# Kernel optimization log

Measured on AMD Instinct MI355X. Metric: run time of the kernel, lower is better.

Reference implementation:

```python
import jax, jax.numpy as jnp
import numpy as np

H_DIM, W_DIM, D_MODEL = 128, 128, 1024
N_HEADS, HEAD_DIM = 16, 64


def setup_inputs() -> dict:
    key = jax.random.key(0)
    ks = jax.random.split(key, 8)
    s = D_MODEL ** -0.5
    return {
        "hidden_state": jax.random.normal(ks[0], (H_DIM, W_DIM, D_MODEL), jnp.float32),
        "attn_mask": jnp.zeros((1, 1, W_DIM, W_DIM), jnp.float32),
        "cos": jax.random.uniform(ks[1], (H_DIM, W_DIM, 1, HEAD_DIM), jnp.float32),
        "sin": jax.random.uniform(ks[2], (H_DIM, W_DIM, 1, HEAD_DIM), jnp.float32),
        "Wq": jax.random.normal(ks[3], (D_MODEL, N_HEADS * HEAD_DIM), jnp.float32) * s,
        "Wk": jax.random.normal(ks[4], (D_MODEL, N_HEADS * HEAD_DIM), jnp.float32) * s,
        "Wv": jax.random.normal(ks[5], (D_MODEL, N_HEADS * HEAD_DIM), jnp.float32) * s,
        "Wo": jax.random.normal(ks[6], (2 * D_MODEL, D_MODEL), jnp.float32) * s,
    }


def _rotate_half(x):
    x1, x2 = jnp.split(x, 2, axis=-1)
    return jnp.concatenate((-x2, x1), axis=-1)


def reference(hidden_state, attn_mask, cos, sin, Wq, Wk, Wv, Wo):
    h, w, d = hidden_state.shape
    Dh = cos.shape[-1]
    nH = d // Dh
    # projections (no bias) + RoPE on q/k
    q = (hidden_state @ Wq).reshape(h, w, nH, Dh)
    k = (hidden_state @ Wk).reshape(h, w, nH, Dh)
    v = (hidden_state @ Wv).reshape(h, w, nH, Dh)
    q = q * cos + _rotate_half(q) * sin
    k = k * cos + _rotate_half(k) * sin
    # NOTE: original divides by sqrt(hidden_size), not sqrt(head_dim)
    scale = jnp.sqrt(jnp.asarray(d, hidden_state.dtype))
    # ---- width attention: (h, w, nH, Dh) -> (h, nH, w, Dh) ----
    qx, kx, vx = (t.transpose(0, 2, 1, 3) for t in (q, k, v))
    sx = jnp.einsum('ahqd,ahkd->ahqk', qx, kx) / scale + attn_mask  # (h, nH, w, w)
    ow = jnp.einsum('ahqk,ahkd->ahqd', jax.nn.softmax(sx, axis=-1), vx)
    w_weights = ow.transpose(0, 2, 1, 3)  # (h, w, nH, Dh)
    # ---- height attention: (h, w, nH, Dh) -> (w, nH, h, Dh) ----
    qy, ky, vy = (t.transpose(1, 2, 0, 3) for t in (q, k, v))
    my = jnp.transpose(attn_mask, (2, 1, 0, 3))
    sy = jnp.einsum('ahqd,ahkd->ahqk', qy, ky) / scale + my  # (w, nH, h, h)
    oh = jnp.einsum('ahqk,ahkd->ahqd', jax.nn.softmax(sy, axis=-1), vy)
    h_weights = oh.transpose(2, 0, 1, 3)  # (h, w, nH, Dh)
    cat = jnp.concatenate([w_weights.reshape(h, w, d), h_weights.reshape(h, w, d)], axis=-1)
    return cat @ Wo
```

## Files before the change

### kernel.cpp

```cpp
#include <hip/hip_runtime.h>

typedef unsigned short u16;
typedef unsigned int   u32;
typedef __bf16 bf16;
typedef bf16  bf16x8 __attribute__((ext_vector_type(8)));
typedef float f32x4  __attribute__((ext_vector_type(4)));

__device__ __forceinline__ u16 bf16u(float f) {
    u32 x = __builtin_bit_cast(u32, f);
    x += 0x7fffu + ((x >> 16) & 1u);
    return (u16)(x >> 16);
}

__device__ __forceinline__ void gl_lds16(const void* g, void* l) {
    __builtin_amdgcn_global_load_lds(
        (const __attribute__((address_space(1))) u32*)g,
        (__attribute__((address_space(3))) u32*)l, 16, 0, 0);
}

__global__ __launch_bounds__(256) void cvt_x_kernel(const float4* __restrict__ in,
                                                    ushort4* __restrict__ out, int n4) {
    int i = blockIdx.x * 256 + threadIdx.x;
    if (i >= n4) return;
    float4 f = in[i];
    ushort4 o;
    o.x = bf16u(f.x); o.y = bf16u(f.y); o.z = bf16u(f.z); o.w = bf16u(f.w);
    out[i] = o;
}

__global__ __launch_bounds__(256) void transp_kernel(const float* __restrict__ W,
                                                     u16* __restrict__ WT,
                                                     int rows, int cols) {
    __shared__ float t[32][33];
    int bx = blockIdx.x * 32, by = blockIdx.y * 32;
    int x = threadIdx.x & 31, y = threadIdx.x >> 5;
#pragma unroll
    for (int i = 0; i < 32; i += 8)
        t[y + i][x] = W[(size_t)(by + y + i) * cols + bx + x];
    __syncthreads();
#pragma unroll
    for (int i = 0; i < 32; i += 8)
        WT[(size_t)(bx + y + i) * rows + by + x] = bf16u(t[x][y + i]);
}

#define GBK 32
__global__ __launch_bounds__(256) void gemm2(
    const u16* __restrict__ A, const u16* __restrict__ BT, void* __restrict__ Cout,
    const float* __restrict__ cosp, const float* __restrict__ sinp,
    int M, int N, int K, int mode)
{
    __shared__ u16 Al[2][128 * GBK];
    __shared__ u16 Bl[2][128 * GBK];
    const int tid = threadIdx.x;
    const int wid = tid >> 6, lane = tid & 63;
    const int nx = gridDim.x;
    const int nwg = nx * gridDim.y;
    const int orig = blockIdx.y * nx + blockIdx.x;
    const int vid = (orig & 7) * (nwg >> 3) + (orig >> 3);
    const int m0 = (vid / nx) << 7, n0 = (vid % nx) << 7;
    const int wr = wid >> 1, wc = wid & 1;
    f32x4 acc[4][4] = {};

    const int srow = (wid << 5) + (lane >> 2);
    const int soff = (lane & 3) << 3;
    const u16* Ag0 = A + (size_t)(m0 + srow) * K + soff;
    const u16* Ag1 = Ag0 + (size_t)16 * K;
    const u16* Bg0 = BT + (size_t)(n0 + srow) * K + soff;
    const u16* Bg1 = Bg0 + (size_t)16 * K;
    const int l0 = (wid << 5) * GBK;
    const int l1 = ((wid << 5) + 16) * GBK;

    const int nt = K >> 5;
    gl_lds16(Ag0, &Al[0][l0]);
    gl_lds16(Ag1, &Al[0][l1]);
    gl_lds16(Bg0, &Bl[0][l0]);
    gl_lds16(Bg1, &Bl[0][l1]);
    __syncthreads();

    int cur = 0;
    for (int t = 0; t < nt; ++t) {
        if (t + 1 < nt) {
            const int k0 = (t + 1) << 5;
            const int nb = cur ^ 1;
            gl_lds16(Ag0 + k0, &Al[nb][l0]);
            gl_lds16(Ag1 + k0, &Al[nb][l1]);
            gl_lds16(Bg0 + k0, &Bl[nb][l0]);
            gl_lds16(Bg1 + k0, &Bl[nb][l1]);
        }
        bf16x8 af[4], bfr[4];
#pragma unroll
        for (int i = 0; i < 4; i++)
            af[i] = *(const bf16x8*)&Al[cur][(((wr << 6) + (i << 4) + (lane & 15)) * GBK) + ((lane >> 4) << 3)];
#pragma unroll
        for (int i = 0; i < 4; i++)
            bfr[i] = *(const bf16x8*)&Bl[cur][(((wc << 6) + (i << 4) + (lane & 15)) * GBK) + ((lane >> 4) << 3)];
#pragma unroll
        for (int mi = 0; mi < 4; mi++)
#pragma unroll
            for (int ni = 0; ni < 4; ni++)
                acc[mi][ni] = __builtin_amdgcn_mfma_f32_16x16x32_bf16(af[mi], bfr[ni], acc[mi][ni], 0, 0, 0);
        __syncthreads();
        cur ^= 1;
    }

    const int colbase = n0 + (wc << 6) + (lane & 15);
    if (mode == 2) {
        float* C = (float*)Cout;
#pragma unroll
        for (int mi = 0; mi < 4; mi++)
#pragma unroll
            for (int r = 0; r < 4; r++) {
                int m = m0 + (wr << 6) + (mi << 4) + ((lane >> 4) << 2) + r;
                float* row = C + (size_t)m * N + colbase;
#pragma unroll
                for (int ni = 0; ni < 4; ni++) row[ni << 4] = acc[mi][ni][r];
            }
    } else if (n0 < 2048) {
        u16* C = (u16*)Cout;
#pragma unroll
        for (int mi = 0; mi < 4; mi++)
#pragma unroll
            for (int r = 0; r < 4; r++) {
                int m = m0 + (wr << 6) + (mi << 4) + ((lane >> 4) << 2) + r;
                const float* cb = cosp + ((size_t)m << 6);
                const float* sb = sinp + ((size_t)m << 6);
                u16* row = C + (size_t)m * N + colbase;
#pragma unroll
                for (int ni = 0; ni < 4; ni++) {
                    int d = (ni << 4) + (lane & 15);
                    float c = cb[d], s = sb[d];
                    float v0 = acc[mi][ni][r];
                    float vr = acc[mi][ni ^ 2][r];
                    float o = fmaf(v0, c, (ni < 2 ? -vr : vr) * s);
                    row[ni << 4] = bf16u(o);
                }
            }
    } else {
        u16* C = (u16*)Cout;
#pragma unroll
        for (int mi = 0; mi < 4; mi++)
#pragma unroll
            for (int r = 0; r < 4; r++) {
                int m = m0 + (wr << 6) + (mi << 4) + ((lane >> 4) << 2) + r;
                u16* row = C + (size_t)m * N + colbase;
#pragma unroll
                for (int ni = 0; ni < 4; ni++) row[ni << 4] = bf16u(acc[mi][ni][r]);
            }
    }
}

__global__ __launch_bounds__(256) void axial_attn(
    const u16* __restrict__ qkv, const float* __restrict__ mask,
    u16* __restrict__ cat, int hmode)
{
    __shared__ u16 Kl[128 * 64];
    __shared__ u16 VT[64 * 128];
    __shared__ u16 Pl[128 * 128];
    const int orig = blockIdx.x;
    const int b = (orig & 7) * 256 + (orig >> 3);
    const int a = b >> 4, hd = b & 15;
    const int tid = threadIdx.x, wid = tid >> 6, lane = tid & 63;
    const int tmul = hmode ? 128 : 1;
    const int tadd = hmode ? a : (a << 7);
    const size_t hoff = (size_t)hd << 6;

#pragma unroll
    for (int c = 0; c < 4; c++) {
        int row = (wid << 5) + (c << 3) + (lane >> 3);
        int sc = (lane & 7) ^ (row & 7);
        gl_lds16(qkv + (size_t)(row * tmul + tadd) * 3072 + 1024 + hoff + (sc << 3),
                 &Kl[((wid << 5) + (c << 3)) << 6]);
    }
#pragma unroll
    for (int i = 0; i < 4; i++) {
        int cid = tid + (i << 8);
        int j = cid >> 3;
        int d0 = (cid & 7) << 3;
        uint4 raw = *(const uint4*)(qkv + (size_t)(j * tmul + tadd) * 3072 + 2048 + hoff + d0);
        const u16* e = (const u16*)&raw;
#pragma unroll
        for (int t = 0; t < 8; t++) {
            int d = d0 + t;
            VT[(d << 7) + (((j >> 3) ^ (d & 15)) << 3) + (j & 7)] = e[t];
        }
    }
    bf16x8 aq[2][2];
#pragma unroll
    for (int qt = 0; qt < 2; qt++)
#pragma unroll
        for (int ks = 0; ks < 2; ks++) {
            int row = (wid << 5) + (qt << 4) + (lane & 15);
            aq[qt][ks] = *(const bf16x8*)(qkv + (size_t)(row * tmul + tadd) * 3072 + hoff
                                          + (ks << 5) + ((lane >> 4) << 3));
        }
    __syncthreads();

    f32x4 S[2][8] = {};
#pragma unroll
    for (int kt = 0; kt < 8; kt++) {
        bf16x8 bk[2];
#pragma unroll
        for (int ks = 0; ks < 2; ks++) {
            int row = (kt << 4) + (lane & 15);
            int ch = ((ks << 2) + (lane >> 4)) ^ (row & 7);
            bk[ks] = *(const bf16x8*)&Kl[(row << 6) + (ch << 3)];
        }
#pragma unroll
        for (int qt = 0; qt < 2; qt++) {
            S[qt][kt] = __builtin_amdgcn_mfma_f32_16x16x32_bf16(aq[qt][0], bk[0], S[qt][kt], 0, 0, 0);
            S[qt][kt] = __builtin_amdgcn_mfma_f32_16x16x32_bf16(aq[qt][1], bk[1], S[qt][kt], 0, 0, 0);
        }
    }

    const float scale = 0.03125f;
#pragma unroll
    for (int qt = 0; qt < 2; qt++) {
#pragma unroll
        for (int r = 0; r < 4; r++) {
            int qrow = (wid << 5) + (qt << 4) + ((lane >> 4) << 2) + r;
            const float* mrow = mask + (hmode ? (a << 7) : (qrow << 7));
            float mx = -1e30f;
#pragma unroll
            for (int kt = 0; kt < 8; kt++) {
                float sv = fmaf(S[qt][kt][r], scale, mrow[(kt << 4) + (lane & 15)]);
                S[qt][kt][r] = sv;
                mx = fmaxf(mx, sv);
            }
            mx = fmaxf(mx, __shfl_xor(mx, 1));
            mx = fmaxf(mx, __shfl_xor(mx, 2));
            mx = fmaxf(mx, __shfl_xor(mx, 4));
            mx = fmaxf(mx, __shfl_xor(mx, 8));
            float sum = 0.f;
#pragma unroll
            for (int kt = 0; kt < 8; kt++) {
                float p = __expf(S[qt][kt][r] - mx);
                S[qt][kt][r] = p;
                sum += p;
            }
            sum += __shfl_xor(sum, 1);
            sum += __shfl_xor(sum, 2);
            sum += __shfl_xor(sum, 4);
            sum += __shfl_xor(sum, 8);
            float rinv = 1.0f / sum;
#pragma unroll
            for (int kt = 0; kt < 8; kt++) {
                int kcol = (kt << 4) + (lane & 15);
                int ch = (kcol >> 3) ^ (qrow & 15);
                Pl[(qrow << 7) + (ch << 3) + (kcol & 7)] = bf16u(S[qt][kt][r] * rinv);
            }
        }
    }
    __syncthreads();

    f32x4 O[4][2] = {};
#pragma unroll
    for (int ks = 0; ks < 4; ks++) {
        bf16x8 av[4], bp[2];
#pragma unroll
        for (int dt = 0; dt < 4; dt++) {
            int drow = (dt << 4) + (lane & 15);
            int ch = ((ks << 2) + (lane >> 4)) ^ (drow & 15);
            av[dt] = *(const bf16x8*)&VT[(drow << 7) + (ch << 3)];
        }
#pragma unroll
        for (int qt = 0; qt < 2; qt++) {
            int qrow = (wid << 5) + (qt << 4) + (lane & 15);
            int ch = ((ks << 2) + (lane >> 4)) ^ (qrow & 15);
            bp[qt] = *(const bf16x8*)&Pl[(qrow << 7) + (ch << 3)];
        }
#pragma unroll
        for (int dt = 0; dt < 4; dt++)
#pragma unroll
            for (int qt = 0; qt < 2; qt++)
                O[dt][qt] = __builtin_amdgcn_mfma_f32_16x16x32_bf16(av[dt], bp[qt], O[dt][qt], 0, 0, 0);
    }

    const int cbase = (hmode ? 1024 : 0) + (hd << 6);
#pragma unroll
    for (int dt = 0; dt < 4; dt++)
#pragma unroll
        for (int qt = 0; qt < 2; qt++) {
            int qrow = (wid << 5) + (qt << 4) + (lane & 15);
            int d0 = (dt << 4) + ((lane >> 4) << 2);
            size_t base = ((size_t)(qrow * tmul + tadd) << 11) + cbase + d0;
            ushort4 pk;
            pk.x = bf16u(O[dt][qt][0]);
            pk.y = bf16u(O[dt][qt][1]);
            pk.z = bf16u(O[dt][qt][2]);
            pk.w = bf16u(O[dt][qt][3]);
            *(ushort4*)(cat + base) = pk;
        }
}

extern "C" void kernel_launch(void* const* d_in, const int* in_sizes, int n_in,
                              void* d_out, int out_size, void* d_ws, size_t ws_size,
                              hipStream_t stream)
{
    (void)in_sizes; (void)n_in; (void)out_size; (void)ws_size;
    const float* hidden = (const float*)d_in[0];
    const float* mask   = (const float*)d_in[1];
    const float* cosp   = (const float*)d_in[2];
    const float* sinp   = (const float*)d_in[3];
    const float* Wq     = (const float*)d_in[4];
    const float* Wk     = (const float*)d_in[5];
    const float* Wv     = (const float*)d_in[6];
    const float* Wo     = (const float*)d_in[7];

    char* ws = (char*)d_ws;
    u16* Xb    = (u16*)(ws);
    u16* WqkvT = (u16*)(ws + 33554432);
    u16* cat   = (u16*)(ws);
    u16* WoT   = (u16*)(ws + 67108864);
    u16* qkvb  = (u16*)(ws + 71303168);

    cvt_x_kernel<<<16384, 256, 0, stream>>>((const float4*)hidden, (ushort4*)Xb, 4194304);

    transp_kernel<<<dim3(32, 32), 256, 0, stream>>>(Wq, WqkvT,               1024, 1024);
    transp_kernel<<<dim3(32, 32), 256, 0, stream>>>(Wk, WqkvT + 1024 * 1024, 1024, 1024);
    transp_kernel<<<dim3(32, 32), 256, 0, stream>>>(Wv, WqkvT + 2048 * 1024, 1024, 1024);
    transp_kernel<<<dim3(32, 64), 256, 0, stream>>>(Wo, WoT, 2048, 1024);

    gemm2<<<dim3(24, 128), 256, 0, stream>>>(Xb, WqkvT, qkvb, cosp, sinp, 16384, 3072, 1024, 1);

    axial_attn<<<2048, 256, 0, stream>>>(qkvb, mask, cat, 0);
    axial_attn<<<2048, 256, 0, stream>>>(qkvb, mask, cat, 1);

    gemm2<<<dim3(8, 128), 256, 0, stream>>>(cat, WoT, d_out, nullptr, nullptr, 16384, 1024, 2048, 2);
}
```

Measured before the change: 366.1 us.

## Replace 128x128 double-buffered GEMM with 256x256 four-stage pipelined GEMM

Swaps the bf16 MFMA GEMM for a version with 256x256 tiles and 8 waves per block. Each wave computes a 128x64 sub-tile. Global-to-LDS loads are staged three iterations ahead in a four-buffer ring, using explicit vmcnt waits and a single barrier per k-step. LDS chunks are XOR-swizzled to cut bank conflicts, and s_setprio is raised around the MFMA burst. The goal is more data reuse per LDS byte and better latency hiding; in exchange it uses about 128KB of LDS per block, more accumulator registers, and fewer blocks (one wave's worth for the output projection).

```diff
diff --git a/kernel.cpp b/kernel.cpp
--- a/kernel.cpp
+++ b/kernel.cpp
@@ -43,74 +43,84 @@
         WT[(size_t)(bx + y + i) * rows + by + x] = bf16u(t[x][y + i]);
 }
 
-#define GBK 32
-__global__ __launch_bounds__(256) void gemm2(
+#define BK2 32
+__global__ __launch_bounds__(512, 2) void gemm8(
     const u16* __restrict__ A, const u16* __restrict__ BT, void* __restrict__ Cout,
     const float* __restrict__ cosp, const float* __restrict__ sinp,
     int M, int N, int K, int mode)
 {
-    __shared__ u16 Al[2][128 * GBK];
-    __shared__ u16 Bl[2][128 * GBK];
+    __shared__ u16 Al[4][256 * BK2];
+    __shared__ u16 Bl[4][256 * BK2];
     const int tid = threadIdx.x;
     const int wid = tid >> 6, lane = tid & 63;
     const int nx = gridDim.x;
     const int nwg = nx * gridDim.y;
     const int orig = blockIdx.y * nx + blockIdx.x;
     const int vid = (orig & 7) * (nwg >> 3) + (orig >> 3);
-    const int m0 = (vid / nx) << 7, n0 = (vid % nx) << 7;
-    const int wr = wid >> 1, wc = wid & 1;
-    f32x4 acc[4][4] = {};
-
-    const int srow = (wid << 5) + (lane >> 2);
-    const int soff = (lane & 3) << 3;
-    const u16* Ag0 = A + (size_t)(m0 + srow) * K + soff;
-    const u16* Ag1 = Ag0 + (size_t)16 * K;
-    const u16* Bg0 = BT + (size_t)(n0 + srow) * K + soff;
-    const u16* Bg1 = Bg0 + (size_t)16 * K;
-    const int l0 = (wid << 5) * GBK;
-    const int l1 = ((wid << 5) + 16) * GBK;
+    const int m0 = (vid / nx) << 8, n0 = (vid % nx) << 8;
+    const int wr = wid >> 2, wc = wid & 3;
+
+    const int c0 = tid, c1 = 512 + tid;
+    const int r0 = c0 >> 2, r1 = c1 >> 2;
+    const int ch0 = (c0 & 3) ^ ((r0 >> 1) & 3);
+    const int ch1 = (c1 & 3) ^ ((r1 >> 1) & 3);
+    const u16* aS0 = A + (size_t)(m0 + r0) * K + (ch0 << 3);
+    const u16* aS1 = A + (size_t)(m0 + r1) * K + (ch1 << 3);
+    const u16* bS0 = BT + (size_t)(n0 + r0) * K + (ch0 << 3);
+    const u16* bS1 = BT + (size_t)(n0 + r1) * K + (ch1 << 3);
+    const int ldsw = wid << 9;
+
+#define STAGE(tt) do { int _b = (tt) & 3; size_t _ko = (size_t)(tt) * BK2; \
+        gl_lds16(aS0 + _ko, &Al[_b][ldsw]);         \
+        gl_lds16(aS1 + _ko, &Al[_b][4096 + ldsw]);  \
+        gl_lds16(bS0 + _ko, &Bl[_b][ldsw]);         \
+        gl_lds16(bS1 + _ko, &Bl[_b][4096 + ldsw]);  } while (0)
 
     const int nt = K >> 5;
-    gl_lds16(Ag0, &Al[0][l0]);
-    gl_lds16(Ag1, &Al[0][l1]);
-    gl_lds16(Bg0, &Bl[0][l0]);
-    gl_lds16(Bg1, &Bl[0][l1]);
-    __syncthreads();
-
-    int cur = 0;
+    STAGE(0); STAGE(1); STAGE(2);
+
+    const int ch_rd = (((lane >> 4) ^ ((lane >> 1) & 3)) << 3);
+    const int ra = (wr << 7) + (lane & 15);
+    const int rb = (wc << 6) + (lane & 15);
+
+    f32x4 acc[8][4] = {};
+
     for (int t = 0; t < nt; ++t) {
-        if (t + 1 < nt) {
-            const int k0 = (t + 1) << 5;
-            const int nb = cur ^ 1;
-            gl_lds16(Ag0 + k0, &Al[nb][l0]);
-            gl_lds16(Ag1 + k0, &Al[nb][l1]);
-            gl_lds16(Bg0 + k0, &Bl[nb][l0]);
-            gl_lds16(Bg1 + k0, &Bl[nb][l1]);
-        }
-        bf16x8 af[4], bfr[4];
-#pragma unroll
-        for (int i = 0; i < 4; i++)
-            af[i] = *(const bf16x8*)&Al[cur][(((wr << 6) + (i << 4) + (lane & 15)) * GBK) + ((lane >> 4) << 3)];
-#pragma unroll
-        for (int i = 0; i < 4; i++)
-            bfr[i] = *(const bf16x8*)&Bl[cur][(((wc << 6) + (i << 4) + (lane & 15)) * GBK) + ((lane >> 4) << 3)];
-#pragma unroll
-        for (int mi = 0; mi < 4; mi++)
+        asm volatile("s_waitcnt lgkmcnt(0)" ::: "memory");
+        if (t + 2 < nt)      asm volatile("s_waitcnt vmcnt(8)" ::: "memory");
+        else if (t + 1 < nt) asm volatile("s_waitcnt vmcnt(4)" ::: "memory");
+        else                 asm volatile("s_waitcnt vmcnt(0)" ::: "memory");
+        __builtin_amdgcn_s_barrier();
+        if (t + 3 < nt) STAGE(t + 3);
+
+        const u16* Ab = &Al[t & 3][0];
+        const u16* Bb = &Bl[t & 3][0];
+        bf16x8 af[8], bfr[4];
+#pragma unroll
+        for (int mi = 0; mi < 8; mi++)
+            af[mi] = *(const bf16x8*)&Ab[((ra + (mi << 4)) << 5) + ch_rd];
+#pragma unroll
+        for (int ni = 0; ni < 4; ni++)
+            bfr[ni] = *(const bf16x8*)&Bb[((rb + (ni << 4)) << 5) + ch_rd];
+
+        __builtin_amdgcn_s_setprio(1);
+#pragma unroll
+        for (int mi = 0; mi < 8; mi++)
 #pragma unroll
             for (int ni = 0; ni < 4; ni++)
                 acc[mi][ni] = __builtin_amdgcn_mfma_f32_16x16x32_bf16(af[mi], bfr[ni], acc[mi][ni], 0, 0, 0);
-        __syncthreads();
-        cur ^= 1;
-    }
+        __builtin_amdgcn_s_setprio(0);
+    }
+#undef STAGE
 
     const int colbase = n0 + (wc << 6) + (lane & 15);
     if (mode == 2) {
         float* C = (float*)Cout;
 #pragma unroll
-        for (int mi = 0; mi < 4; mi++)
+        for (int mi = 0; mi < 8; mi++)
 #pragma unroll
             for (int r = 0; r < 4; r++) {
-                int m = m0 + (wr << 6) + (mi << 4) + ((lane >> 4) << 2) + r;
+                int m = m0 + (wr << 7) + (mi << 4) + ((lane >> 4) << 2) + r;
                 float* row = C + (size_t)m * N + colbase;
 #pragma unroll
                 for (int ni = 0; ni < 4; ni++) row[ni << 4] = acc[mi][ni][r];
@@ -118,10 +128,10 @@
     } else if (n0 < 2048) {
         u16* C = (u16*)Cout;
 #pragma unroll
-        for (int mi = 0; mi < 4; mi++)
+        for (int mi = 0; mi < 8; mi++)
 #pragma unroll
             for (int r = 0; r < 4; r++) {
-                int m = m0 + (wr << 6) + (mi << 4) + ((lane >> 4) << 2) + r;
+                int m = m0 + (wr << 7) + (mi << 4) + ((lane >> 4) << 2) + r;
                 const float* cb = cosp + ((size_t)m << 6);
                 const float* sb = sinp + ((size_t)m << 6);
                 u16* row = C + (size_t)m * N + colbase;
@@ -138,10 +148,10 @@
     } else {
         u16* C = (u16*)Cout;
 #pragma unroll
-        for (int mi = 0; mi < 4; mi++)
+        for (int mi = 0; mi < 8; mi++)
 #pragma unroll
             for (int r = 0; r < 4; r++) {
-                int m = m0 + (wr << 6) + (mi << 4) + ((lane >> 4) << 2) + r;
+                int m = m0 + (wr << 7) + (mi << 4) + ((lane >> 4) << 2) + r;
                 u16* row = C + (size_t)m * N + colbase;
 #pragma unroll
                 for (int ni = 0; ni < 4; ni++) row[ni << 4] = bf16u(acc[mi][ni][r]);
@@ -320,10 +330,10 @@
     transp_kernel<<<dim3(32, 32), 256, 0, stream>>>(Wv, WqkvT + 2048 * 1024, 1024, 1024);
     transp_kernel<<<dim3(32, 64), 256, 0, stream>>>(Wo, WoT, 2048, 1024);
 
-    gemm2<<<dim3(24, 128), 256, 0, stream>>>(Xb, WqkvT, qkvb, cosp, sinp, 16384, 3072, 1024, 1);
+    gemm8<<<dim3(12, 64), 512, 0, stream>>>(Xb, WqkvT, qkvb, cosp, sinp, 16384, 3072, 1024, 1);
 
     axial_attn<<<2048, 256, 0, stream>>>(qkvb, mask, cat, 0);
     axial_attn<<<2048, 256, 0, stream>>>(qkvb, mask, cat, 1);
 
-    gemm2<<<dim3(8, 128), 256, 0, stream>>>(cat, WoT, d_out, nullptr, nullptr, 16384, 1024, 2048, 2);
-}
+    gemm8<<<dim3(4, 64), 512, 0, stream>>>(cat, WoT, d_out, nullptr, nullptr, 16384, 1024, 2048, 2);
+}
```

After: 362.0 us. Within noise of the previous version (-1.1%).
